# Optimization experiments

Measured on AMD Instinct MI355X. Metric: run time of the kernel, lower is better.

Reference implementation:

```python
import jax, jax.numpy as jnp
import numpy as np

jax.config.update("jax_enable_x64", True)

B = 16384          # batch size (rows of features)
K = 256            # num_unlabel (clusters)
EPS = 0.05         # sinkhorn epsilon
GAMMA = 5.0        # KL regularizer weight
LR = 0.1           # SGD lr for w
MOM = 0.99         # SGD momentum
N_INNER = 3        # sinkhorn iterations
N_OUTER = 10       # outer optimization iterations


def setup_inputs() -> dict:
    key = jax.random.key(0)
    features = jax.random.normal(key, (B, K), dtype=jnp.float32)
    w = jnp.ones((1, K), dtype=jnp.float32) / K  # torch Parameter init: ones/K
    return {"features": features, "w": w, "head": 0}


def _sinkhorn(logits, w):
    """SinkhornKnopp_im.forward: logits [B,K] -> Q [B,K] (float64), preds=logits64."""
    logits64 = logits.astype(jnp.float64)
    Q = jnp.exp(logits64 / EPS).T            # [K, B]
    Q = Q / jnp.sum(Q)
    K2 = jax.nn.softmax(w, axis=1).astype(jnp.float64)  # [1, K] marginal prior
    Bn = Q.shape[1]
    for _ in range(N_INNER):
        Q = Q / jnp.sum(Q, axis=1, keepdims=True)       # row normalize
        Q = Q * K2.T                                    # scale rows by prior
        Q = Q / jnp.sum(Q, axis=0, keepdims=True)       # column normalize
        Q = Q / Bn
    Q = Q * Bn
    return Q.T, logits64                                # [B, K], [B, K]


def _total_loss(w, features):
    Q, preds = _sinkhorn(features, w)
    loss = -jnp.mean(jnp.sum(Q * preds, axis=1))
    # KLDivLoss(batchmean): input = log_softmax(w).T [K,1], target = softmax(w0).T = 1/K
    logw = jax.nn.log_softmax(w, axis=1)[0]             # [K]
    t = jnp.float32(1.0 / K)
    reg = jnp.sum(t * (jnp.log(t) - logw)) / K
    return loss + GAMMA * reg.astype(jnp.float64), Q


def reference(features, w, head):
    features = jax.lax.stop_gradient(features)  # features.detach()

    def step(carry, _):
        w, buf, _ = carry
        (_, Q), g = jax.value_and_grad(_total_loss, has_aux=True)(w, features)
        # clip_grad_norm_(params, 1)
        norm = jnp.sqrt(jnp.sum(g.astype(jnp.float64) ** 2)).astype(g.dtype)
        g = g * jnp.minimum(jnp.float32(1.0), jnp.float32(1.0) / (norm + 1e-6))
        # SGD with momentum 0.99 (buf starts at 0 -> first buf = g, matching torch)
        buf = MOM * buf + g
        w = w - LR * buf
        return (w, buf, Q), None

    Q0 = jnp.zeros((features.shape[0], K), dtype=jnp.float64)
    (w_f, buf_f, Q), _ = jax.lax.scan(
        step, (w, jnp.zeros_like(w), Q0), None, length=N_OUTER
    )
    return Q  # Q from the last outer iteration (computed with pre-update w)
```

## Files before the change

kernel.cpp:

```cpp
#include <hip/hip_runtime.h>


namespace {

constexpr int KDIM = 256;
constexpr int NBLK = 256;
constexpr int ROWS = 64;
constexpr int NRED = 16;
constexpr float L2E20 = 28.853900817779268f;

constexpr size_t P_DBL   = 2ull * 256 * 512;
constexpr size_t FIN_OFF = P_DBL;
constexpr size_t FIN_PAR = 6ull * 16 * 256 * 2;
constexpr size_t FIN_DBL = 2 * FIN_PAR;
constexpr size_t FLAG_OFF_DBL = FIN_OFF + FIN_DBL;
constexpr int FLAG_U32 = 256 * 32;

__device__ __forceinline__ double fast_exp_d(double x) {
  const double LOG2E  = 1.4426950408889634074;
  const double LN2_HI = 6.93147180369123816490e-01;
  const double LN2_LO = 1.90821492927058770002e-10;
  double n = rint(x * LOG2E);
  double t = fma(-n, LN2_HI, x);
  t = fma(-n, LN2_LO, t);
  double p = 2.4801587301587302e-05;
  p = fma(p, t, 1.9841269841269841e-04);
  p = fma(p, t, 1.3888888888888889e-03);
  p = fma(p, t, 8.3333333333333333e-03);
  p = fma(p, t, 4.1666666666666664e-02);
  p = fma(p, t, 1.6666666666666666e-01);
  p = fma(p, t, 0.5);
  p = fma(p, t, 1.0);
  p = fma(p, t, 1.0);
  long long ni = (long long)n;
  double s = __longlong_as_double((unsigned long long)(ni + 1023LL) << 52);
  return p * s;
}

__device__ __forceinline__ double wave_sum_d(double v) {
#pragma unroll
  for (int o = 32; o > 0; o >>= 1) v += __shfl_down(v, o);
  return v;
}
__device__ __forceinline__ double wave_max_d(double v) {
#pragma unroll
  for (int o = 32; o > 0; o >>= 1) v = fmax(v, __shfl_down(v, o));
  return v;
}

__device__ __forceinline__ double pload(const double* p) {
  return __hip_atomic_load(p, __ATOMIC_RELAXED, __HIP_MEMORY_SCOPE_AGENT);
}
__device__ __forceinline__ void pstore(double* p, double v) {
  __hip_atomic_store(p, v, __ATOMIC_RELAXED, __HIP_MEMORY_SCOPE_AGENT);
}

}

__global__ __launch_bounds__(256) void kInitWS(double* __restrict__ ws) {
  const double QN = __builtin_nan("");
  size_t gid = (size_t)blockIdx.x * 256 + threadIdx.x;
  size_t stride = (size_t)gridDim.x * 256;
  double* fin = ws + FIN_OFF;
  for (size_t j = gid; j < FIN_DBL; j += stride) fin[j] = QN;
  unsigned* fl = (unsigned*)(ws + FLAG_OFF_DBL);
  if (gid < FLAG_U32) fl[gid] = 0u;
}

__global__ __launch_bounds__(256, 1) void sink_main(
    const float* __restrict__ feat, const float* __restrict__ w_in,
    float* __restrict__ out, double* __restrict__ ws) {
  __shared__ float  Et[ROWS * KDIM];
  __shared__ float  Ft[ROWS * KDIM];
  __shared__ double alpha[KDIM];
  __shared__ double tmp1[KDIM];
  __shared__ double tmp2[KDIM];
  __shared__ double sfin[32];
  __shared__ double v1s[ROWS], v2s[ROWS], v3s[ROWS];
  __shared__ double grow[ROWS], wrow[ROWS], sbr[ROWS];
  __shared__ float  mrow[ROWS];
  __shared__ double sred[8];

  const int t = threadIdx.x, bid = blockIdx.x;
  const int wv = t >> 6, lane = t & 63;
  const int b0 = bid * ROWS;
  const double QN = __builtin_nan("");

  double* P = ws;
  double* fin = ws + FIN_OFF;
  unsigned* flag1 = (unsigned*)(ws + FLAG_OFF_DBL);

  auto blk_sum = [&](double v) -> double {
    v = wave_sum_d(v);
    __syncthreads();
    if (lane == 0) sred[wv] = v;
    __syncthreads();
    return sred[0] + sred[1] + sred[2] + sred[3];
  };
  auto blk_max = [&](double v) -> double {
    v = wave_max_d(v);
    __syncthreads();
    if (lane == 0) sred[wv + 4] = v;
    __syncthreads();
    return fmax(fmax(sred[4], sred[5]), fmax(sred[6], sred[7]));
  };

  auto allreduce = [&](unsigned ph, int kind, bool pair, int par,
                       double pa, double pb, double& r1, double& r2) {
    double* row = P + (((size_t)(ph & 1)) * 256 + bid) * 512;
    pstore(&row[2 * t], pa);
    if (pair) pstore(&row[2 * t + 1], pb);
    __syncthreads();
    if (t == 0)
      __hip_atomic_store(&flag1[bid * 32], ph, __ATOMIC_RELAXED,
                         __HIP_MEMORY_SCOPE_AGENT);
    if (bid < NRED) {
      const int rep = t >> 4, c = t & 15;
      {
        double* dst = fin + (size_t)(1 - par) * FIN_PAR +
                      (size_t)kind * 8192 + (size_t)rep * 512 +
                      2 * (size_t)(bid * 16 + c);
        pstore(dst, QN);
        pstore(dst + 1, QN);
      }
      {
        const unsigned* f = &flag1[t * 32];
        while (__hip_atomic_load(f, __ATOMIC_RELAXED,
                                 __HIP_MEMORY_SCOPE_AGENT) < ph)
          __builtin_amdgcn_s_sleep(1);
      }
      __syncthreads();
      const double* base = P + ((size_t)(ph & 1)) * 131072;
      const int k = bid * 16 + c;
      double a1 = 0.0, a2 = 0.0;
#pragma unroll
      for (int i = 0; i < 16; ++i) {
        const double* rr = base + (size_t)(rep + 16 * i) * 512;
        a1 += pload(&rr[2 * k]);
        if (pair) a2 += pload(&rr[2 * k + 1]);
      }
      tmp1[t] = a1;
      if (pair) tmp2[t] = a2;
      __syncthreads();
      if (t < 16) {
        double s = 0.0;
#pragma unroll
        for (int g2 = 0; g2 < 16; ++g2) s += tmp1[g2 * 16 + t];
        sfin[2 * t] = s;
        if (!pair) sfin[2 * t + 1] = 0.0;
      } else if (pair && t < 32) {
        int c2 = t - 16;
        double s = 0.0;
#pragma unroll
        for (int g2 = 0; g2 < 16; ++g2) s += tmp2[g2 * 16 + c2];
        sfin[2 * c2 + 1] = s;
      }
      __syncthreads();
      {
        double* dst = fin + (size_t)par * FIN_PAR + (size_t)kind * 8192 +
                      (size_t)rep * 512 + 2 * (size_t)(bid * 16 + c);
        pstore(dst, sfin[2 * c]);
        if (pair) pstore(dst + 1, sfin[2 * c + 1]);
      }
    }
    {
      const double* e = fin + (size_t)par * FIN_PAR + (size_t)kind * 8192 +
                        (size_t)(bid & 15) * 512 + 2 * (size_t)t;
      double a;
      for (;;) {
        a = pload(e);
        if (!__builtin_isnan(a)) break;
        __builtin_amdgcn_s_sleep(1);
      }
      r1 = a;
      if (pair) {
        double b;
        for (;;) {
          b = pload(e + 1);
          if (!__builtin_isnan(b)) break;
          __builtin_amdgcn_s_sleep(1);
        }
        r2 = b;
      }
    }
    __syncthreads();
  };

  auto row_pass = [&](double* dstv) {
    double a0 = alpha[4 * lane + 0], a1 = alpha[4 * lane + 1];
    double a2 = alpha[4 * lane + 2], a3 = alpha[4 * lane + 3];
#pragma unroll 4
    for (int r = wv; r < ROWS; r += 4) {
      float4 e4 = ((const float4*)(Et + r * KDIM))[lane];
      double s1 = a0 * (double)e4.x + a1 * (double)e4.y +
                  a2 * (double)e4.z + a3 * (double)e4.w;
      s1 = wave_sum_d(s1);
      if (lane == 0) dstv[r] = s1;
    }
  };
  auto col_partial = [&]() -> double {
    double a = 0.0;
#pragma unroll 8
    for (int r = 0; r < ROWS; ++r) a += (double)Et[r * KDIM + t] * wrow[r];
    return a;
  };

  {
    const float4* src = (const float4*)(feat + (size_t)b0 * KDIM);
    float4* dst = (float4*)Ft;
#pragma unroll
    for (int s = 0; s < 16; ++s) dst[s * 256 + t] = src[s * 256 + t];
  }
  __syncthreads();
  for (int r = wv; r < ROWS; r += 4) {
    float4 f4 = ((const float4*)(Ft + r * KDIM))[lane];
    float m = fmaxf(fmaxf(f4.x, f4.y), fmaxf(f4.z, f4.w));
#pragma unroll
    for (int o = 32; o > 0; o >>= 1) m = fmaxf(m, __shfl_down(m, o));
    if (lane == 0) {
      mrow[r] = m;
      sbr[r] = fast_exp_d(20.0 * (double)m);
    }
  }
  __syncthreads();
  double pu0 = 0.0;
#pragma unroll 8
  for (int r = 0; r < ROWS; ++r) {
    float e = exp2f((Ft[r * KDIM + t] - mrow[r]) * L2E20);
    Et[r * KDIM + t] = e;
    pu0 += (double)e * sbr[r];
  }
  float w_t = w_in[t], buf_t = 0.0f;
  double k2_t;
  {
    double x = (double)w_t;
    double m = blk_max(x);
    double e = fast_exp_d(x - m);
    double s = blk_sum(e);
    k2_t = e / s;
  }
  unsigned ph = 1;
  double u0_t, dmy;
  allreduce(ph, 0, false, 0, pu0, 0.0, u0_t, dmy);

  for (int it = 0; it < 10; ++it) {
    const int p = it & 1;
    double u1_t, u2_t;

    alpha[t] = k2_t / u0_t;
    __syncthreads();
    row_pass(v1s);
    __syncthreads();
    if (t < ROWS) wrow[t] = 1.0 / (16384.0 * v1s[t]);
    __syncthreads();
    {
      double pa = col_partial();
      ++ph; allreduce(ph, 1, false, p, pa, 0.0, u1_t, dmy);
    }

    alpha[t] = k2_t / u1_t;
    __syncthreads();
    row_pass(v2s);
    __syncthreads();
    if (t < ROWS) wrow[t] = 1.0 / (16384.0 * v2s[t]);
    __syncthreads();
    {
      double pa = col_partial();
      ++ph; allreduce(ph, 2, false, p, pa, 0.0, u2_t, dmy);
    }

    if (it == 9) {
      alpha[t] = k2_t / u2_t;
      __syncthreads();
      row_pass(v3s);
      __syncthreads();
      if (t < ROWS) wrow[t] = 1.0 / v3s[t];
      __syncthreads();
      double a3 = alpha[t];
#pragma unroll 4
      for (int r = 0; r < ROWS; ++r)
        out[(size_t)(b0 + r) * KDIM + t] =
            (float)(a3 * (double)Et[r * KDIM + t] * wrow[r]);
      return;
    }

    alpha[t] = k2_t / u2_t;
    __syncthreads();
    {
      double a0 = alpha[4 * lane + 0], a1 = alpha[4 * lane + 1];
      double a2 = alpha[4 * lane + 2], a3 = alpha[4 * lane + 3];
#pragma unroll 2
      for (int r = wv; r < ROWS; r += 4) {
        float4 e4 = ((const float4*)(Et + r * KDIM))[lane];
        float4 f4 = ((const float4*)(Ft + r * KDIM))[lane];
        double p0 = a0 * (double)e4.x, p1 = a1 * (double)e4.y;
        double p2 = a2 * (double)e4.z, p3 = a3 * (double)e4.w;
        double s1 = p0 + p1 + p2 + p3;
        double s2 = p0 * (double)f4.x + p1 * (double)f4.y +
                    p2 * (double)f4.z + p3 * (double)f4.w;
        s1 = wave_sum_d(s1);
        s2 = wave_sum_d(s2);
        if (lane == 0) {
          v3s[r] = s1;
          grow[r] = s2 / (16384.0 * s1 * s1);
        }
      }
    }
    __syncthreads();
    if (t < ROWS) wrow[t] = -1.0 / (16384.0 * v3s[t]);
    __syncthreads();
    double gd_t, t3_t;
    {
      double ac1 = 0.0, ac2 = 0.0;
#pragma unroll 8
      for (int r = 0; r < ROWS; ++r) {
        double ed = (double)Et[r * KDIM + t];
        ac1 += ed * (double)Ft[r * KDIM + t] * wrow[r];
        ac2 += ed * grow[r];
      }
      ++ph; allreduce(ph, 3, true, p, ac1, ac2, gd_t, t3_t);
    }

    alpha[t] = -(gd_t + t3_t) * k2_t / (u2_t * u2_t);
    __syncthreads();
    row_pass(grow);
    __syncthreads();
    if (t < ROWS) wrow[t] = -grow[t] / (16384.0 * v2s[t] * v2s[t]);
    __syncthreads();
    double ga2_t;
    {
      double pa = col_partial();
      ++ph; allreduce(ph, 4, false, p, pa, 0.0, ga2_t, dmy);
    }

    alpha[t] = -ga2_t * k2_t / (u1_t * u1_t);
    __syncthreads();
    row_pass(grow);
    __syncthreads();
    if (t < ROWS) wrow[t] = -grow[t] / (16384.0 * v1s[t] * v1s[t]);
    __syncthreads();
    double ga1_t;
    {
      double pa = col_partial();
      ++ph; allreduce(ph, 5, false, p, pa, 0.0, ga1_t, dmy);
    }

    {
      double gk2 = (gd_t + t3_t) / u2_t + ga2_t / u1_t + ga1_t / u0_t;
      double dot = blk_sum(k2_t * gk2);
      double gw = k2_t * (gk2 - dot) + 5.0 * (k2_t / 256.0 - 1.0 / 65536.0);
      double n2 = blk_sum(gw * gw);
      float normf = (float)sqrt(n2);
      float sc = fminf(1.0f, 1.0f / (normf + 1e-6f));
      float g = (float)gw * sc;
      buf_t = 0.99f * buf_t + g;
      w_t = w_t - 0.1f * buf_t;
      double x = (double)w_t;
      double m = blk_max(x);
      double e = fast_exp_d(x - m);
      double s = blk_sum(e);
      k2_t = e / s;
    }
  }
}

extern "C" void kernel_launch(void* const* d_in, const int* in_sizes, int n_in,
                              void* d_out, int out_size, void* d_ws,
                              size_t ws_size, hipStream_t stream) {
  (void)in_sizes; (void)n_in; (void)out_size; (void)ws_size;
  const float* feat = (const float*)d_in[0];
  const float* w_in = (const float*)d_in[1];
  float* out = (float*)d_out;
  double* ws = (double*)d_ws;

  kInitWS<<<128, 256, 0, stream>>>(ws);
  sink_main<<<NBLK, 256, 0, stream>>>(feat, w_in, out, ws);
}
```

Measured before the change: 558.1 us.

## Dedicate reducer blocks and replace flag barriers with NaN-sentinel polling

Splits the 256-block persistent grid into 16 dedicated reducer blocks and 240 worker blocks that now own 68 or 69 rows each, instead of every block doing both jobs. The separate per-block arrival flags are dropped: workers publish partials into NaN-initialised slots and reset them afterwards, and reducers poll each slot until it becomes non-NaN. This is meant to take reduction work and a barrier off the workers' critical path at each of the many grid-wide allreduces. In exchange, workers carry more rows each, and the sentinel protocol relies on NaN never appearing as a real partial value and on the ordering of the reset stores.

```diff
diff --git a/kernel.cpp b/kernel.cpp
--- a/kernel.cpp
+++ b/kernel.cpp
@@ -5,16 +5,16 @@
 
 constexpr int KDIM = 256;
 constexpr int NBLK = 256;
-constexpr int ROWS = 64;
 constexpr int NRED = 16;
+constexpr int NW   = 240;
+constexpr int RMAX = 69;
 constexpr float L2E20 = 28.853900817779268f;
 
-constexpr size_t P_DBL   = 2ull * 256 * 512;
+constexpr size_t P_DBL   = 2ull * NW * 512;
 constexpr size_t FIN_OFF = P_DBL;
-constexpr size_t FIN_PAR = 6ull * 16 * 256 * 2;
+constexpr size_t FIN_PAR = 6ull * 16 * 512;
 constexpr size_t FIN_DBL = 2 * FIN_PAR;
-constexpr size_t FLAG_OFF_DBL = FIN_OFF + FIN_DBL;
-constexpr int FLAG_U32 = 256 * 32;
+constexpr size_t WS_DBL  = P_DBL + FIN_DBL;
 
 __device__ __forceinline__ double fast_exp_d(double x) {
   const double LOG2E  = 1.4426950408889634074;
@@ -61,34 +61,102 @@
   const double QN = __builtin_nan("");
   size_t gid = (size_t)blockIdx.x * 256 + threadIdx.x;
   size_t stride = (size_t)gridDim.x * 256;
-  double* fin = ws + FIN_OFF;
-  for (size_t j = gid; j < FIN_DBL; j += stride) fin[j] = QN;
-  unsigned* fl = (unsigned*)(ws + FLAG_OFF_DBL);
-  if (gid < FLAG_U32) fl[gid] = 0u;
+  for (size_t j = gid; j < WS_DBL; j += stride) ws[j] = QN;
 }
 
 __global__ __launch_bounds__(256, 1) void sink_main(
     const float* __restrict__ feat, const float* __restrict__ w_in,
     float* __restrict__ out, double* __restrict__ ws) {
-  __shared__ float  Et[ROWS * KDIM];
-  __shared__ float  Ft[ROWS * KDIM];
+  __shared__ float  Et[RMAX * KDIM];
+  __shared__ float  Ft[RMAX * KDIM];
   __shared__ double alpha[KDIM];
   __shared__ double tmp1[KDIM];
   __shared__ double tmp2[KDIM];
   __shared__ double sfin[32];
-  __shared__ double v1s[ROWS], v2s[ROWS], v3s[ROWS];
-  __shared__ double grow[ROWS], wrow[ROWS], sbr[ROWS];
-  __shared__ float  mrow[ROWS];
+  __shared__ double v1s[RMAX], v2s[RMAX], v3s[RMAX];
+  __shared__ double grow[RMAX], wrow[RMAX], sbr[RMAX];
+  __shared__ float  mrow[RMAX];
   __shared__ double sred[8];
 
   const int t = threadIdx.x, bid = blockIdx.x;
   const int wv = t >> 6, lane = t & 63;
-  const int b0 = bid * ROWS;
   const double QN = __builtin_nan("");
 
   double* P = ws;
   double* fin = ws + FIN_OFF;
-  unsigned* flag1 = (unsigned*)(ws + FLAG_OFF_DBL);
+
+  if (bid < NRED) {
+    const int rep = t >> 4, c = t & 15;
+    const int k = bid * 16 + c;
+
+    auto do_reduce = [&](unsigned ph, int kind, bool pair, int par) {
+      const int q = ph & 1;
+      if (kind != 0) {
+        double* dst = fin + (size_t)(1 - par) * FIN_PAR +
+                      (size_t)kind * 8192 + (size_t)rep * 512 + k;
+        pstore(dst, QN);
+        if (pair) pstore(dst + 256, QN);
+      }
+      double a1 = 0.0, a2 = 0.0;
+      unsigned m1 = 0x7FFFu, m2 = pair ? 0x7FFFu : 0u;
+      while (m1 | m2) {
+#pragma unroll
+        for (int i = 0; i < 15; ++i) {
+          const double* e = P + ((size_t)q * NW + (rep + 16 * i)) * 512 + k;
+          if ((m1 >> i) & 1u) {
+            double v = pload(e);
+            if (!__builtin_isnan(v)) { a1 += v; m1 &= ~(1u << i); }
+          }
+          if ((m2 >> i) & 1u) {
+            double v = pload(e + 256);
+            if (!__builtin_isnan(v)) { a2 += v; m2 &= ~(1u << i); }
+          }
+        }
+        if (m1 | m2) __builtin_amdgcn_s_sleep(1);
+      }
+      tmp1[t] = a1;
+      if (pair) tmp2[t] = a2;
+      __syncthreads();
+      if (t < 16) {
+        double s = 0.0;
+#pragma unroll
+        for (int g = 0; g < 16; ++g) s += tmp1[g * 16 + t];
+        sfin[t] = s;
+      } else if (pair && t < 32) {
+        const int c2 = t - 16;
+        double s = 0.0;
+#pragma unroll
+        for (int g = 0; g < 16; ++g) s += tmp2[g * 16 + c2];
+        sfin[16 + c2] = s;
+      }
+      __syncthreads();
+      {
+        double* dst = fin + (size_t)par * FIN_PAR + (size_t)kind * 8192 +
+                      (size_t)rep * 512 + k;
+        pstore(dst, sfin[c]);
+        if (pair) pstore(dst + 256, sfin[16 + c]);
+      }
+      __syncthreads();
+    };
+
+    unsigned ph = 1;
+    do_reduce(ph, 0, false, 0);
+    for (int it = 0; it < 9; ++it) {
+      const int par = it & 1;
+      ++ph; do_reduce(ph, 1, false, par);
+      ++ph; do_reduce(ph, 2, false, par);
+      ++ph; do_reduce(ph, 3, true,  par);
+      ++ph; do_reduce(ph, 4, false, par);
+      ++ph; do_reduce(ph, 5, false, par);
+    }
+    ++ph; do_reduce(ph, 1, false, 1);
+    ++ph; do_reduce(ph, 2, false, 1);
+    return;
+  }
+
+  const int wid = bid - NRED;
+  const int nr = (wid < 64) ? 69 : 68;
+  const int start = (wid < 64) ? wid * 69 : 4416 + (wid - 64) * 68;
 
   auto blk_sum = [&](double v) -> double {
     v = wave_sum_d(v);
@@ -105,92 +173,37 @@
     return fmax(fmax(sred[4], sred[5]), fmax(sred[6], sred[7]));
   };
 
-  auto allreduce = [&](unsigned ph, int kind, bool pair, int par,
-                       double pa, double pb, double& r1, double& r2) {
-    double* row = P + (((size_t)(ph & 1)) * 256 + bid) * 512;
-    pstore(&row[2 * t], pa);
-    if (pair) pstore(&row[2 * t + 1], pb);
-    __syncthreads();
-    if (t == 0)
-      __hip_atomic_store(&flag1[bid * 32], ph, __ATOMIC_RELAXED,
-                         __HIP_MEMORY_SCOPE_AGENT);
-    if (bid < NRED) {
-      const int rep = t >> 4, c = t & 15;
-      {
-        double* dst = fin + (size_t)(1 - par) * FIN_PAR +
-                      (size_t)kind * 8192 + (size_t)rep * 512 +
-                      2 * (size_t)(bid * 16 + c);
-        pstore(dst, QN);
-        pstore(dst + 1, QN);
-      }
-      {
-        const unsigned* f = &flag1[t * 32];
-        while (__hip_atomic_load(f, __ATOMIC_RELAXED,
-                                 __HIP_MEMORY_SCOPE_AGENT) < ph)
-          __builtin_amdgcn_s_sleep(1);
-      }
-      __syncthreads();
-      const double* base = P + ((size_t)(ph & 1)) * 131072;
-      const int k = bid * 16 + c;
-      double a1 = 0.0, a2 = 0.0;
-#pragma unroll
-      for (int i = 0; i < 16; ++i) {
-        const double* rr = base + (size_t)(rep + 16 * i) * 512;
-        a1 += pload(&rr[2 * k]);
-        if (pair) a2 += pload(&rr[2 * k + 1]);
-      }
-      tmp1[t] = a1;
-      if (pair) tmp2[t] = a2;
-      __syncthreads();
-      if (t < 16) {
-        double s = 0.0;
-#pragma unroll
-        for (int g2 = 0; g2 < 16; ++g2) s += tmp1[g2 * 16 + t];
-        sfin[2 * t] = s;
-        if (!pair) sfin[2 * t + 1] = 0.0;
-      } else if (pair && t < 32) {
-        int c2 = t - 16;
-        double s = 0.0;
-#pragma unroll
-        for (int g2 = 0; g2 < 16; ++g2) s += tmp2[g2 * 16 + c2];
-        sfin[2 * c2 + 1] = s;
-      }
-      __syncthreads();
-      {
-        double* dst = fin + (size_t)par * FIN_PAR + (size_t)kind * 8192 +
-                      (size_t)rep * 512 + 2 * (size_t)(bid * 16 + c);
-        pstore(dst, sfin[2 * c]);
-        if (pair) pstore(dst + 1, sfin[2 * c + 1]);
-      }
-    }
-    {
-      const double* e = fin + (size_t)par * FIN_PAR + (size_t)kind * 8192 +
-                        (size_t)(bid & 15) * 512 + 2 * (size_t)t;
-      double a;
+  auto w_allreduce = [&](unsigned ph, int kind, bool pair, int par,
+                         double pa, double pb, double& r1, double& r2) {
+    const int q = ph & 1;
+    double* row = P + ((size_t)q * NW + wid) * 512;
+    pstore(&row[t], pa);
+    if (pair) pstore(&row[256 + t], pb);
+    const double* e = fin + (size_t)par * FIN_PAR + (size_t)kind * 8192 +
+                      (size_t)(wid & 15) * 512 + t;
+    double a;
+    for (;;) {
+      a = pload(e);
+      if (!__builtin_isnan(a)) break;
+      __builtin_amdgcn_s_sleep(1);
+    }
+    r1 = a;
+    if (pair) {
       for (;;) {
-        a = pload(e);
-        if (!__builtin_isnan(a)) break;
+        double b2 = pload(e + 256);
+        if (!__builtin_isnan(b2)) { r2 = b2; break; }
         __builtin_amdgcn_s_sleep(1);
       }
-      r1 = a;
-      if (pair) {
-        double b;
-        for (;;) {
-          b = pload(e + 1);
-          if (!__builtin_isnan(b)) break;
-          __builtin_amdgcn_s_sleep(1);
-        }
-        r2 = b;
-      }
-    }
-    __syncthreads();
+    }
+    __syncthreads();
+    pstore(&row[t], QN);
+    pstore(&row[256 + t], QN);
   };
 
   auto row_pass = [&](double* dstv) {
     double a0 = alpha[4 * lane + 0], a1 = alpha[4 * lane + 1];
     double a2 = alpha[4 * lane + 2], a3 = alpha[4 * lane + 3];
-#pragma unroll 4
-    for (int r = wv; r < ROWS; r += 4) {
+    for (int r = wv; r < nr; r += 4) {
       float4 e4 = ((const float4*)(Et + r * KDIM))[lane];
       double s1 = a0 * (double)e4.x + a1 * (double)e4.y +
                   a2 * (double)e4.z + a3 * (double)e4.w;
@@ -200,19 +213,19 @@
   };
   auto col_partial = [&]() -> double {
     double a = 0.0;
-#pragma unroll 8
-    for (int r = 0; r < ROWS; ++r) a += (double)Et[r * KDIM + t] * wrow[r];
+#pragma unroll 4
+    for (int r = 0; r < nr; ++r) a += (double)Et[r * KDIM + t] * wrow[r];
     return a;
   };
 
   {
-    const float4* src = (const float4*)(feat + (size_t)b0 * KDIM);
+    const float4* src = (const float4*)(feat + (size_t)start * KDIM);
     float4* dst = (float4*)Ft;
-#pragma unroll
-    for (int s = 0; s < 16; ++s) dst[s * 256 + t] = src[s * 256 + t];
+    const int total4 = nr * 64;
+    for (int s = t; s < total4; s += 256) dst[s] = src[s];
   }
   __syncthreads();
-  for (int r = wv; r < ROWS; r += 4) {
+  for (int r = wv; r < nr; r += 4) {
     float4 f4 = ((const float4*)(Ft + r * KDIM))[lane];
     float m = fmaxf(fmaxf(f4.x, f4.y), fmaxf(f4.z, f4.w));
 #pragma unroll
@@ -224,8 +237,8 @@
   }
   __syncthreads();
   double pu0 = 0.0;
-#pragma unroll 8
-  for (int r = 0; r < ROWS; ++r) {
+#pragma unroll 4
+  for (int r = 0; r < nr; ++r) {
     float e = exp2f((Ft[r * KDIM + t] - mrow[r]) * L2E20);
     Et[r * KDIM + t] = e;
     pu0 += (double)e * sbr[r];
@@ -241,7 +254,7 @@
   }
   unsigned ph = 1;
   double u0_t, dmy;
-  allreduce(ph, 0, false, 0, pu0, 0.0, u0_t, dmy);
+  w_allreduce(ph, 0, false, 0, pu0, 0.0, u0_t, dmy);
 
   for (int it = 0; it < 10; ++it) {
     const int p = it & 1;
@@ -251,35 +264,29 @@
     __syncthreads();
     row_pass(v1s);
     __syncthreads();
-    if (t < ROWS) wrow[t] = 1.0 / (16384.0 * v1s[t]);
-    __syncthreads();
-    {
-      double pa = col_partial();
-      ++ph; allreduce(ph, 1, false, p, pa, 0.0, u1_t, dmy);
-    }
+    if (t < nr) wrow[t] = 1.0 / (16384.0 * v1s[t]);
+    __syncthreads();
+    { double pa = col_partial(); ++ph; w_allreduce(ph, 1, false, p, pa, 0.0, u1_t, dmy); }
 
     alpha[t] = k2_t / u1_t;
     __syncthreads();
     row_pass(v2s);
     __syncthreads();
-    if (t < ROWS) wrow[t] = 1.0 / (16384.0 * v2s[t]);
-    __syncthreads();
-    {
-      double pa = col_partial();
-      ++ph; allreduce(ph, 2, false, p, pa, 0.0, u2_t, dmy);
-    }
+    if (t < nr) wrow[t] = 1.0 / (16384.0 * v2s[t]);
+    __syncthreads();
+    { double pa = col_partial(); ++ph; w_allreduce(ph, 2, false, p, pa, 0.0, u2_t, dmy); }
 
     if (it == 9) {
       alpha[t] = k2_t / u2_t;
       __syncthreads();
       row_pass(v3s);
       __syncthreads();
-      if (t < ROWS) wrow[t] = 1.0 / v3s[t];
+      if (t < nr) wrow[t] = 1.0 / v3s[t];
       __syncthreads();
       double a3 = alpha[t];
 #pragma unroll 4
-      for (int r = 0; r < ROWS; ++r)
-        out[(size_t)(b0 + r) * KDIM + t] =
+      for (int r = 0; r < nr; ++r)
+        out[(size_t)(start + r) * KDIM + t] =
             (float)(a3 * (double)Et[r * KDIM + t] * wrow[r]);
       return;
     }
@@ -289,8 +296,7 @@
     {
       double a0 = alpha[4 * lane + 0], a1 = alpha[4 * lane + 1];
       double a2 = alpha[4 * lane + 2], a3 = alpha[4 * lane + 3];
-#pragma unroll 2
-      for (int r = wv; r < ROWS; r += 4) {
+      for (int r = wv; r < nr; r += 4) {
         float4 e4 = ((const float4*)(Et + r * KDIM))[lane];
         float4 f4 = ((const float4*)(Ft + r * KDIM))[lane];
         double p0 = a0 * (double)e4.x, p1 = a1 * (double)e4.y;
@@ -307,43 +313,37 @@
       }
     }
     __syncthreads();
-    if (t < ROWS) wrow[t] = -1.0 / (16384.0 * v3s[t]);
+    if (t < nr) wrow[t] = -1.0 / (16384.0 * v3s[t]);
     __syncthreads();
     double gd_t, t3_t;
     {
       double ac1 = 0.0, ac2 = 0.0;
-#pragma unroll 8
-      for (int r = 0; r < ROWS; ++r) {
+#pragma unroll 4
+      for (int r = 0; r < nr; ++r) {
         double ed = (double)Et[r * KDIM + t];
         ac1 += ed * (double)Ft[r * KDIM + t] * wrow[r];
         ac2 += ed * grow[r];
       }
-      ++ph; allreduce(ph, 3, true, p, ac1, ac2, gd_t, t3_t);
+      ++ph; w_allreduce(ph, 3, true, p, ac1, ac2, gd_t, t3_t);
     }
 
     alpha[t] = -(gd_t + t3_t) * k2_t / (u2_t * u2_t);
     __syncthreads();
     row_pass(grow);
     __syncthreads();
-    if (t < ROWS) wrow[t] = -grow[t] / (16384.0 * v2s[t] * v2s[t]);
+    if (t < nr) wrow[t] = -grow[t] / (16384.0 * v2s[t] * v2s[t]);
     __syncthreads();
     double ga2_t;
-    {
-      double pa = col_partial();
-      ++ph; allreduce(ph, 4, false, p, pa, 0.0, ga2_t, dmy);
-    }
+    { double pa = col_partial(); ++ph; w_allreduce(ph, 4, false, p, pa, 0.0, ga2_t, dmy); }
 
     alpha[t] = -ga2_t * k2_t / (u1_t * u1_t);
     __syncthreads();
     row_pass(grow);
     __syncthreads();
-    if (t < ROWS) wrow[t] = -grow[t] / (16384.0 * v1s[t] * v1s[t]);
+    if (t < nr) wrow[t] = -grow[t] / (16384.0 * v1s[t] * v1s[t]);
     __syncthreads();
     double ga1_t;
-    {
-      double pa = col_partial();
-      ++ph; allreduce(ph, 5, false, p, pa, 0.0, ga1_t, dmy);
-    }
+    { double pa = col_partial(); ++ph; w_allreduce(ph, 5, false, p, pa, 0.0, ga1_t, dmy); }
 
     {
       double gk2 = (gd_t + t3_t) / u2_t + ga2_t / u1_t + ga1_t / u0_t;
```

Result: slower. 808.2 us (+44.8%).
